# Performance work log

Hardware: AMD Instinct MI355X
Metric: run time of the kernel (lower is better)

Reference implementation:

```python
import jax, jax.numpy as jnp
import numpy as np

B = 64; SEQ = 512; PRED = 96; D = 321; HID = 2048
WIN = 64; STRIDE = WIN // 2; FT = WIN // 2 + 1
LOW = int(FT * 0.3); MID = int(FT * 0.4); HIGH = FT - LOW - MID  # 9, 13, 11
NW = SEQ // STRIDE + 1; EMBED = NW * WIN  # 17, 1088
EPS = 1e-5; SCALE = 0.02
LH = int(LOW * 2.0); MH = int(MID * 2.0); HH = int(HIGH * 2.0)  # 18, 26, 22


def _clayer(key, fan_in, fan_out):
    k1, k2, k3, k4 = jax.random.split(key, 4)
    return (jax.random.normal(k1, (fan_in, fan_out), jnp.float32) * SCALE,
            jax.random.normal(k2, (fan_in, fan_out), jnp.float32) * SCALE,
            jax.random.normal(k3, (fan_out,), jnp.float32) * SCALE,
            jax.random.normal(k4, (fan_out,), jnp.float32) * SCALE)


def setup_inputs() -> dict:
    key = jax.random.key(0)
    ks = jax.random.split(key, 12)
    inp = {}
    inp["x"] = jax.random.normal(ks[0], (B, SEQ, D), jnp.float32)
    inp["x_mark_enc"] = jax.random.normal(ks[1], (B, SEQ, 4), jnp.float32)
    inp["x_dec"] = jax.random.normal(ks[2], (B, PRED, D), jnp.float32)
    inp["x_mark_dec"] = jax.random.normal(ks[3], (B, PRED, 4), jnp.float32)
    n = jnp.arange(WIN, dtype=jnp.float32)
    inp["window"] = 0.5 * (1.0 - jnp.cos(2.0 * jnp.pi * n / WIN))  # torch.hann_window (periodic)
    inp["revin_w"] = jnp.ones((D,), jnp.float32)
    inp["revin_b"] = jnp.zeros((D,), jnp.float32)
    # low band filter: 3 complex layers LOW->LH->LH->LOW
    for i, (fi, fo) in enumerate([(LOW, LH), (LH, LH), (LH, LOW)]):
        wr, wi, br, bi = _clayer(jax.random.fold_in(ks[4], i), fi, fo)
        inp[f"low{i}_wr"], inp[f"low{i}_wi"], inp[f"low{i}_br"], inp[f"low{i}_bi"] = wr, wi, br, bi
    # mid band filter: 2 complex layers MID->MH->MID
    for i, (fi, fo) in enumerate([(MID, MH), (MH, MID)]):
        wr, wi, br, bi = _clayer(jax.random.fold_in(ks[5], i), fi, fo)
        inp[f"mid{i}_wr"], inp[f"mid{i}_wi"], inp[f"mid{i}_br"], inp[f"mid{i}_bi"] = wr, wi, br, bi
    # high band filter: 1 complex layer HIGH->HIGH
    wr, wi, br, bi = _clayer(ks[6], HIGH, HIGH)
    inp["high0_wr"], inp["high0_wi"], inp["high0_br"], inp["high0_bi"] = wr, wi, br, bi
    inp["fc1_w"] = jax.random.normal(ks[7], (EMBED, HID), jnp.float32) * SCALE
    inp["fc1_b"] = jnp.zeros((HID,), jnp.float32)
    inp["fc2_w"] = jax.random.normal(ks[8], (HID, PRED), jnp.float32) * SCALE
    inp["fc2_b"] = jnp.zeros((PRED,), jnp.float32)
    return inp


def _clin(z, wr, wi, br, bi):
    return z @ (wr + 1j * wi) + (br + 1j * bi)


def _cact(z):
    return jax.nn.leaky_relu(z.real) + 1j * jax.nn.leaky_relu(z.imag)


def reference(x, x_mark_enc, x_dec, x_mark_dec, window, revin_w, revin_b,
              low0_wr, low0_wi, low0_br, low0_bi,
              low1_wr, low1_wi, low1_br, low1_bi,
              low2_wr, low2_wi, low2_br, low2_bi,
              mid0_wr, mid0_wi, mid0_br, mid0_bi,
              mid1_wr, mid1_wi, mid1_br, mid1_bi,
              high0_wr, high0_wi, high0_br, high0_bi,
              fc1_w, fc1_b, fc2_w, fc2_b):
    # RevIN norm over time dim
    mean = jnp.mean(x, axis=1, keepdims=True)
    std = jnp.sqrt(jnp.var(x, axis=1, keepdims=True) + EPS)
    xn = (x - mean) / std * revin_w + revin_b
    xc = jnp.transpose(xn, (0, 2, 1))                      # [B, D, L]
    xp = jnp.pad(xc, ((0, 0), (0, 0), (STRIDE, STRIDE)))
    # batched window extraction (replaces python loop over windows)
    idx = jnp.arange(NW)[:, None] * STRIDE + jnp.arange(WIN)[None, :]
    seg = xp[:, :, idx]
    w = window / jnp.linalg.norm(window)
    xf = jnp.fft.rfft(seg * w, axis=-1)                    # [B, D, NW, FT] complex
    low = xf[..., :LOW]
    mid = xf[..., LOW:LOW + MID]
    high = xf[..., LOW + MID:]
    low = _clin(_cact(_clin(_cact(_clin(low, low0_wr, low0_wi, low0_br, low0_bi)),
                            low1_wr, low1_wi, low1_br, low1_bi)),
                low2_wr, low2_wi, low2_br, low2_bi)
    mid = _clin(_cact(_clin(mid, mid0_wr, mid0_wi, mid0_br, mid0_bi)),
                mid1_wr, mid1_wi, mid1_br, mid1_bi)
    high = _clin(high, high0_wr, high0_wi, high0_br, high0_bi)
    xfil = jnp.concatenate([low, mid, high], axis=-1)      # [B, D, NW, FT]
    xt = jnp.fft.irfft(xfil, n=WIN, axis=-1)
    emb = xt.reshape(x.shape[0], D, EMBED)
    h = jax.nn.leaky_relu(emb @ fc1_w + fc1_b)
    y = h @ fc2_w + fc2_b                                  # [B, D, PRED]
    y = jnp.transpose(y, (0, 2, 1))                        # [B, PRED, D]
    # RevIN denorm
    y = (y - revin_b) / (revin_w + EPS * EPS) * std + mean
    return y
```

## Files before the change

### kernel.cpp

```cpp
#include <hip/hip_runtime.h>

typedef unsigned short u16;
typedef unsigned int   u32;
typedef __attribute__((ext_vector_type(4))) float  fvec4;
typedef __attribute__((ext_vector_type(8))) __bf16 bvec8;

#define NB    64
#define SEQL  512
#define DCH   321
#define BDTOT (NB * DCH)
#define NWIN  17
#define PREDL 96
#define MWTOT (BDTOT * NWIN)

__device__ __forceinline__ u16 f2bf(float f) {
    union { float f; u32 u; } v; v.f = f;
    u32 r = v.u + 0x7FFFu + ((v.u >> 16) & 1u);
    return (u16)(r >> 16);
}
__device__ __forceinline__ float lrelu(float v) { return v > 0.f ? v : 0.01f * v; }

__device__ __forceinline__ void gld16(const u16* g, u16* l) {
    __builtin_amdgcn_global_load_lds((const __attribute__((address_space(1))) void*)g,
                                     (__attribute__((address_space(3))) void*)l, 16, 0, 0);
}

__global__ __launch_bounds__(256) void stats_kernel(const float* __restrict__ x,
                                                    float* __restrict__ mean,
                                                    float* __restrict__ rstd,
                                                    float* __restrict__ stdv) {
    __shared__ float ls[2][4][64];
    int i = threadIdx.x & 63;
    int j = threadIdx.x >> 6;
    int bd = blockIdx.x * 64 + i;
    int b = bd / DCH, d = bd - b * DCH;
    float s = 0.f, ss = 0.f;
    for (int t = j; t < SEQL; t += 4) {
        float v = x[((size_t)b * SEQL + t) * DCH + d];
        s += v; ss += v * v;
    }
    ls[0][j][i] = s; ls[1][j][i] = ss;
    __syncthreads();
    if (j == 0) {
        s  = ls[0][0][i] + ls[0][1][i] + ls[0][2][i] + ls[0][3][i];
        ss = ls[1][0][i] + ls[1][1][i] + ls[1][2][i] + ls[1][3][i];
        float m   = s * (1.f / SEQL);
        float var = ss * (1.f / SEQL) - m * m;
        float st  = sqrtf(var + 1e-5f);
        mean[bd] = m; rstd[bd] = 1.f / st; stdv[bd] = st;
    }
}

__global__ __launch_bounds__(256) void norm_transpose(const float* __restrict__ x,
                                                      const float* __restrict__ mean,
                                                      const float* __restrict__ rstd,
                                                      const float* __restrict__ rw,
                                                      const float* __restrict__ rb,
                                                      u16* __restrict__ xnT) {
    __shared__ float tile[64][65];
    int d0 = blockIdx.x * 64, s0 = blockIdx.y * 64, b = blockIdx.z;
    for (int e = threadIdx.x; e < 4096; e += 256) {
        int sr = e >> 6, dc = e & 63;
        int d = d0 + dc;
        tile[sr][dc] = (d < DCH) ? x[((size_t)b * SEQL + s0 + sr) * DCH + d] : 0.f;
    }
    __syncthreads();
    for (int e = threadIdx.x; e < 4096; e += 256) {
        int dr = e >> 6, sc = e & 63;
        int d = d0 + dr;
        if (d < DCH) {
            int bd = b * DCH + d;
            float v = (tile[sc][dr] - mean[bd]) * rstd[bd] * rw[d] + rb[d];
            xnT[(size_t)bd * 576 + 32 + s0 + sc] = f2bf(v);
        }
    }
}

__global__ __launch_bounds__(256) void pad_zero(u16* __restrict__ xnT) {
    int idx = blockIdx.x * 256 + threadIdx.x;
    if (idx < BDTOT * 64) {
        int bd = idx >> 6, q = idx & 63;
        int off = q < 32 ? q : 512 + q;
        xnT[(size_t)bd * 576 + off] = 0;
    }
}

__global__ __launch_bounds__(256) void precompute_kernel(
    const float* __restrict__ window,
    const float* __restrict__ l0wr, const float* __restrict__ l0wi,
    const float* __restrict__ l0br, const float* __restrict__ l0bi,
    const float* __restrict__ l1wr, const float* __restrict__ l1wi,
    const float* __restrict__ l1br, const float* __restrict__ l1bi,
    const float* __restrict__ l2wr, const float* __restrict__ l2wi,
    const float* __restrict__ l2br, const float* __restrict__ l2bi,
    const float* __restrict__ m0wr, const float* __restrict__ m0wi,
    const float* __restrict__ m0br, const float* __restrict__ m0bi,
    const float* __restrict__ m1wr, const float* __restrict__ m1wi,
    const float* __restrict__ m1br, const float* __restrict__ m1bi,
    const float* __restrict__ h0wr, const float* __restrict__ h0wi,
    const float* __restrict__ h0br, const float* __restrict__ h0bi,
    u16* __restrict__ A1t, u16* __restrict__ W1t, u16* __restrict__ B2t,
    float* __restrict__ bias1, float* __restrict__ bias2, float* __restrict__ biast)
{
    int idx = blockIdx.x * 256 + threadIdx.x;
    float nrm = 0.f;
    for (int i = 0; i < 64; ++i) nrm += window[i] * window[i];
    float inv = 1.0f / sqrtf(nrm);
    const float STEP = 6.283185307179586f / 64.f;
    auto Cc = [&](int n, int k) { return  window[n] * inv * cosf(STEP * (float)((k * n) & 63)); };
    auto Ss = [&](int n, int k) { return -window[n] * inv * sinf(STEP * (float)((k * n) & 63)); };
    auto aRe = [&](int k, int n) {
        float sc = (k == 0 || k == 32) ? (1.f / 64.f) : (2.f / 64.f);
        return sc * cosf(STEP * (float)((k * n) & 63));
    };
    auto aIm = [&](int k, int n) {
        if (k == 0 || k == 32) return 0.f;
        return -(2.f / 64.f) * sinf(STEP * (float)((k * n) & 63));
    };
    if (idx < 16384) {
        int j = idx >> 6, n = idx & 63;
        float v = 0.f;
        if (j < 18)                    { for (int k = 0; k < 9;  ++k) v += Cc(n,k)   *l0wr[k*18+j]      - Ss(n,k)   *l0wi[k*18+j]; }
        else if (j < 36)               { int jj=j-18; for (int k = 0; k < 9;  ++k) v += Cc(n,k)   *l0wi[k*18+jj] + Ss(n,k)   *l0wr[k*18+jj]; }
        else if (j >= 64  && j < 90)   { int jj=j-64; for (int k = 0; k < 13; ++k) v += Cc(n,9+k) *m0wr[k*26+jj] - Ss(n,9+k) *m0wi[k*26+jj]; }
        else if (j >= 90  && j < 116)  { int jj=j-90; for (int k = 0; k < 13; ++k) v += Cc(n,9+k) *m0wi[k*26+jj] + Ss(n,9+k) *m0wr[k*26+jj]; }
        else if (j >= 128 && j < 139)  { int jj=j-128;for (int k = 0; k < 11; ++k) v += Cc(n,22+k)*h0wr[k*11+jj] - Ss(n,22+k)*h0wi[k*11+jj]; }
        else if (j >= 139 && j < 150)  { int jj=j-139;for (int k = 0; k < 11; ++k) v += Cc(n,22+k)*h0wi[k*11+jj] + Ss(n,22+k)*h0wr[k*11+jj]; }
        A1t[idx] = f2bf(v);
    } else if (idx < 24576) {
        int t = idx - 16384; int j = t >> 6, k = t & 63;
        float v = 0.f;
        if (j < 18)      { if (k < 18) v = l1wr[k*18+j];        else if (k < 36) v = -l1wi[(k-18)*18+j]; }
        else if (j < 36) { int jj=j-18; if (k < 18) v = l1wi[k*18+jj]; else if (k < 36) v =  l1wr[(k-18)*18+jj]; }
        W1t[t] = f2bf(v);
    } else if (idx < 49152) {
        int t = idx - 24576; int n = t / 192, c = t - n * 192;
        float v = 0.f;
        if (n < 64) {
            if (c < 18)                  { for (int m = 0; m < 9;  ++m) v +=  l2wr[c*9+m]     *aRe(m,n)   + l2wi[c*9+m]     *aIm(m,n); }
            else if (c < 36)             { int cc=c-18; for (int m = 0; m < 9;  ++m) v += -l2wi[cc*9+m]   *aRe(m,n)   + l2wr[cc*9+m]   *aIm(m,n); }
            else if (c >= 64 && c < 90)  { int cc=c-64; for (int m = 0; m < 13; ++m) v +=  m1wr[cc*13+m]  *aRe(9+m,n) + m1wi[cc*13+m]  *aIm(9+m,n); }
            else if (c >= 90 && c < 116) { int cc=c-90; for (int m = 0; m < 13; ++m) v += -m1wi[cc*13+m]  *aRe(9+m,n) + m1wr[cc*13+m]  *aIm(9+m,n); }
            else if (c >= 128 && c < 139){ v = aRe(22 + (c-128), n); }
            else if (c >= 139 && c < 150){ v = aIm(22 + (c-139), n); }
        }
        B2t[t] = f2bf(v);
    } else if (idx < 49344) {
        int c = idx - 49152;
        float v = 0.f;
        if (c < 18) v = l0br[c];
        else if (c < 36) v = l0bi[c-18];
        else if (c >= 64 && c < 90) v = m0br[c-64];
        else if (c >= 90 && c < 116) v = m0bi[c-90];
        bias1[c] = v;
    } else if (idx < 49472) {
        int c = idx - 49344;
        float v = 0.f;
        if (c < 18) v = l1br[c]; else if (c < 36) v = l1bi[c-18];
        bias2[c] = v;
    } else if (idx < 49536) {
        int n = idx - 49472;
        float v = 0.f;
        for (int k = 0; k <= 32; ++k) {
            float br = (k < 9) ? l2br[k] : (k < 22 ? m1br[k-9] : h0br[k-22]);
            float bi = (k < 9) ? l2bi[k] : (k < 22 ? m1bi[k-9] : h0bi[k-22]);
            v += aRe(k, n) * br + aIm(k, n) * bi;
        }
        biast[n] = v;
    }
}

__global__ __launch_bounds__(256) void wtrans(const float* __restrict__ W, u16* __restrict__ Wt,
                                              int R, int C, int Cpad) {
    __shared__ float t[32][33];
    int c0 = blockIdx.x * 32, r0 = blockIdx.y * 32;
    for (int e = threadIdx.x; e < 1024; e += 256) {
        int rr = e >> 5, cc = e & 31;
        int rg = r0 + rr, cg = c0 + cc;
        t[rr][cc] = (rg < R && cg < C) ? W[(size_t)rg * C + cg] : 0.f;
    }
    __syncthreads();
    for (int e = threadIdx.x; e < 1024; e += 256) {
        int cr = e >> 5, rc = e & 31;
        int cg = c0 + cr, rg = r0 + rc;
        if (cg < Cpad && rg < R) Wt[(size_t)cg * R + rg] = f2bf(t[rc][cr]);
    }
}

__global__ __launch_bounds__(256) void spectral_fused(
    const u16* __restrict__ xnT, const u16* __restrict__ A1t,
    const u16* __restrict__ W1t, const u16* __restrict__ B2t,
    const float* __restrict__ bias1, const float* __restrict__ bias2,
    const float* __restrict__ biast, u16* __restrict__ EMB)
{
    __shared__ u16 XB[64 * 72];
    __shared__ u16 ACT[64 * 208];
    const int tid  = threadIdx.x;
    const int lane = tid & 63;
    const int wn   = tid >> 6;
    const int r0   = blockIdx.x * 64;

    {
        int rr = tid >> 2;
        int cc = (tid & 3) * 16;
        u32 gr = (u32)(r0 + rr);
        u32 bd = gr / 17u, nw = gr - bd * 17u;
        const u16* src = xnT + (size_t)bd * 576 + nw * 32 + cc;
        *(bvec8*)&XB[rr * 72 + cc]     = *(const bvec8*)(src);
        *(bvec8*)&XB[rr * 72 + cc + 8] = *(const bvec8*)(src + 8);
    }
    __syncthreads();

    fvec4 acc1[4][3] = {};
#pragma unroll
    for (int kk = 0; kk < 2; ++kk) {
        int ko = kk * 32 + ((lane >> 4) << 3);
        bvec8 af[4], bf[3];
#pragma unroll
        for (int m = 0; m < 4; ++m)
            af[m] = *(const bvec8*)&XB[(m * 16 + (lane & 15)) * 72 + ko];
#pragma unroll
        for (int n = 0; n < 3; ++n)
            bf[n] = *(const bvec8*)(A1t + (size_t)(wn * 48 + n * 16 + (lane & 15)) * 64 + ko);
#pragma unroll
        for (int m = 0; m < 4; ++m)
#pragma unroll
            for (int n = 0; n < 3; ++n)
                acc1[m][n] = __builtin_amdgcn_mfma_f32_16x16x32_bf16(af[m], bf[n], acc1[m][n], 0, 0, 0);
    }
#pragma unroll
    for (int n = 0; n < 3; ++n) {
        int col = wn * 48 + n * 16 + (lane & 15);
        float bs = bias1[col];
#pragma unroll
        for (int m = 0; m < 4; ++m)
#pragma unroll
            for (int q = 0; q < 4; ++q) {
                int row = m * 16 + ((lane >> 4) << 2) + q;
                float v = acc1[m][n][q] + bs;
                if (col < 128) v = lrelu(v);
                ACT[row * 208 + col] = f2bf(v);
            }
    }
    __syncthreads();

    fvec4 acc2[4] = {};
#pragma unroll
    for (int kk = 0; kk < 2; ++kk) {
        int ko = kk * 32 + ((lane >> 4) << 3);
        bvec8 bf = *(const bvec8*)(W1t + (size_t)(wn * 16 + (lane & 15)) * 64 + ko);
#pragma unroll
        for (int m = 0; m < 4; ++m) {
            bvec8 af = *(const bvec8*)&ACT[(m * 16 + (lane & 15)) * 208 + ko];
            acc2[m] = __builtin_amdgcn_mfma_f32_16x16x32_bf16(af, bf, acc2[m], 0, 0, 0);
        }
    }
    __syncthreads();
    {
        int col = wn * 16 + (lane & 15);
        float bs = bias2[col];
#pragma unroll
        for (int m = 0; m < 4; ++m)
#pragma unroll
            for (int q = 0; q < 4; ++q) {
                int row = m * 16 + ((lane >> 4) << 2) + q;
                ACT[row * 208 + col] = f2bf(lrelu(acc2[m][q] + bs));
            }
    }
    __syncthreads();

    fvec4 acc3[4] = {};
#pragma unroll
    for (int kk = 0; kk < 6; ++kk) {
        int ko = kk * 32 + ((lane >> 4) << 3);
        bvec8 bf = *(const bvec8*)(B2t + (size_t)(wn * 16 + (lane & 15)) * 192 + ko);
#pragma unroll
        for (int m = 0; m < 4; ++m) {
            bvec8 af = *(const bvec8*)&ACT[(m * 16 + (lane & 15)) * 208 + ko];
            acc3[m] = __builtin_amdgcn_mfma_f32_16x16x32_bf16(af, bf, acc3[m], 0, 0, 0);
        }
    }
    {
        int col = wn * 16 + (lane & 15);
        float bs = biast[col];
#pragma unroll
        for (int m = 0; m < 4; ++m)
#pragma unroll
            for (int q = 0; q < 4; ++q) {
                int row = m * 16 + ((lane >> 4) << 2) + q;
                EMB[(size_t)(r0 + row) * 64 + col] = f2bf(acc3[m][q] + bs);
            }
    }
}

template <int SWZ>
__global__ __launch_bounds__(512, 2) void gemm256(
    const u16* __restrict__ A, const u16* __restrict__ Bt,
    const float* __restrict__ bias, u16* __restrict__ C,
    int Mloc, int K, int ldc, long long a_off, int nwg)
{
    extern __shared__ u16 lds[];
    const int tid  = threadIdx.x;
    const int lane = tid & 63;
    const int wid  = tid >> 6;
    const int wm   = wid >> 2;
    const int wn   = wid & 3;
    int wg;
    if (SWZ) {
        int bid = blockIdx.x;
        int q = nwg >> 3, r = nwg & 7, xcd = bid & 7, off = bid >> 3;
        wg = (xcd < r) ? (xcd * (q + 1) + off) : (r * (q + 1) + (xcd - r) * q + off);
    } else wg = blockIdx.x;
    const int mt = wg >> 3;
    const int nt = wg & 7;
    const int bm0 = mt * 256, bn0 = nt * 256;

    auto stage = [&](int bufb, int kt) {
        u16* dstA = lds + bufb * 32768;
        u16* dstB = dstA + 16384;
#pragma unroll
        for (int j = 0; j < 4; ++j) {
            int idx = j * 512 + tid;
            int r  = idx >> 3;
            int kc = (idx & 7) << 3;
            int rl = bm0 + r; if (rl > Mloc - 1) rl = Mloc - 1;
            gld16(A  + (size_t)(a_off + rl) * K + kt + kc, dstA + idx * 8);
            gld16(Bt + (size_t)(bn0 + r)   * K + kt + kc, dstB + idx * 8);
        }
    };

    fvec4 acc[8][4] = {};

    auto compute = [&](int bufb) {
        const u16* Ab = lds + bufb * 32768;
        const u16* Bb = Ab + 16384;
        __builtin_amdgcn_s_setprio(1);
#pragma unroll
        for (int kk = 0; kk < 2; ++kk) {
            int ko = kk * 32 + ((lane >> 4) << 3);
            bvec8 af[8], bf[4];
#pragma unroll
            for (int m = 0; m < 8; ++m)
                af[m] = *(const bvec8*)&Ab[(wm * 128 + m * 16 + (lane & 15)) * 64 + ko];
#pragma unroll
            for (int n = 0; n < 4; ++n)
                bf[n] = *(const bvec8*)&Bb[(wn * 64 + n * 16 + (lane & 15)) * 64 + ko];
#pragma unroll
            for (int m = 0; m < 8; ++m)
#pragma unroll
                for (int n = 0; n < 4; ++n)
                    acc[m][n] = __builtin_amdgcn_mfma_f32_16x16x32_bf16(af[m], bf[n], acc[m][n], 0, 0, 0);
        }
        __builtin_amdgcn_s_setprio(0);
    };

    const int NT = K >> 6;
    stage(0, 0);
    int cur = 0;
    for (int t = 0; t < NT - 1; ++t) {
        stage(cur ^ 1, (t + 1) << 6);
        asm volatile("s_waitcnt vmcnt(8)" ::: "memory");
        __builtin_amdgcn_sched_barrier(0);
        __builtin_amdgcn_s_barrier();
        __builtin_amdgcn_sched_barrier(0);
        compute(cur);
        __builtin_amdgcn_sched_barrier(0);
        __builtin_amdgcn_s_barrier();
        __builtin_amdgcn_sched_barrier(0);
        cur ^= 1;
    }
    asm volatile("s_waitcnt vmcnt(0)" ::: "memory");
    __builtin_amdgcn_sched_barrier(0);
    __builtin_amdgcn_s_barrier();
    __builtin_amdgcn_sched_barrier(0);
    compute(cur);

#pragma unroll
    for (int m = 0; m < 8; ++m) {
        int rl0 = bm0 + wm * 128 + m * 16 + ((lane >> 4) << 2);
#pragma unroll
        for (int n = 0; n < 4; ++n) {
            int col = bn0 + wn * 64 + n * 16 + (lane & 15);
            float bs = bias[col];
#pragma unroll
            for (int q = 0; q < 4; ++q) {
                int rl = rl0 + q;
                if (rl < Mloc)
                    C[(size_t)rl * (size_t)ldc + col] = f2bf(lrelu(acc[m][n][q] + bs));
            }
        }
    }
}

__global__ __launch_bounds__(256) void gemm_bt_splitk(
    const u16* __restrict__ A, const u16* __restrict__ Bt,
    void* __restrict__ Cp, int Mloc, int N, int K, int lda, int ldc,
    long long c_off, int klen, long long pstride)
{
    const int tid  = threadIdx.x;
    const int lane = tid & 63;
    const int wm   = (tid >> 7) & 1;
    const int wn   = (tid >> 6) & 1;
    const int mt = blockIdx.y;
    int k0 = blockIdx.x * klen;
    int k1 = (k0 + klen > K) ? K : k0 + klen;
    const int bn0 = 0;
    const int bm0 = mt * 128;
    __shared__ u16 Als[128 * 64];
    __shared__ u16 Bls[128 * 64];
    fvec4 acc[4][4] = {};

    for (int kt = k0; kt < k1; kt += 64) {
#pragma unroll
        for (int i = 0; i < 4; ++i) {
            int idx = i * 256 + tid;
            int r  = idx >> 3;
            int kc = (idx & 7) << 3;
            int rl = bm0 + r; if (rl > Mloc - 1) rl = Mloc - 1;
            gld16(A + (size_t)rl * lda + kt + kc, &Als[idx * 8]);
            gld16(Bt + (size_t)(bn0 + r) * K + kt + kc, &Bls[idx * 8]);
        }
        __syncthreads();
#pragma unroll
        for (int kk = 0; kk < 2; ++kk) {
            int ko = kk * 32 + ((lane >> 4) << 3);
            bvec8 af[4], bfr[4];
#pragma unroll
            for (int m = 0; m < 4; ++m)
                af[m] = *(const bvec8*)&Als[(wm * 64 + m * 16 + (lane & 15)) * 64 + ko];
#pragma unroll
            for (int n = 0; n < 4; ++n)
                bfr[n] = *(const bvec8*)&Bls[(wn * 64 + n * 16 + (lane & 15)) * 64 + ko];
#pragma unroll
            for (int m = 0; m < 4; ++m)
#pragma unroll
                for (int n = 0; n < 4; ++n)
                    acc[m][n] = __builtin_amdgcn_mfma_f32_16x16x32_bf16(af[m], bfr[n], acc[m][n], 0, 0, 0);
        }
        __syncthreads();
    }

#pragma unroll
    for (int m = 0; m < 4; ++m) {
        int rbase = bm0 + wm * 64 + m * 16 + ((lane >> 4) << 2);
#pragma unroll
        for (int n = 0; n < 4; ++n) {
            int col = bn0 + wn * 64 + n * 16 + (lane & 15);
            if (col < N) {
#pragma unroll
                for (int q = 0; q < 4; ++q) {
                    int rl = rbase + q;
                    if (rl < Mloc) {
                        float* yp = (float*)Cp + (size_t)blockIdx.x * pstride;
                        yp[(size_t)(c_off + rl) * ldc + col] = acc[m][n][q];
                    }
                }
            }
        }
    }
}

__global__ __launch_bounds__(256) void final_denorm(const float* __restrict__ YP,
                                                    const float* __restrict__ fc2b,
                                                    const float* __restrict__ mean,
                                                    const float* __restrict__ stdv,
                                                    const float* __restrict__ rw,
                                                    const float* __restrict__ rb,
                                                    float* __restrict__ out) {
    const long long PART = (long long)BDTOT * PREDL;
    __shared__ float t[32][33];
    int d0 = blockIdx.x * 32, p0 = blockIdx.y * 32, b = blockIdx.z;
    for (int e = threadIdx.x; e < 1024; e += 256) {
        int di = e >> 5, pj = e & 31;
        int d = d0 + di, p = p0 + pj;
        if (d < DCH && p < PREDL) {
            size_t off = ((size_t)b * DCH + d) * PREDL + p;
            t[di][pj] = YP[off] + YP[off + PART] + YP[off + 2 * PART] + fc2b[p];
        } else t[di][pj] = 0.f;
    }
    __syncthreads();
    for (int e = threadIdx.x; e < 1024; e += 256) {
        int pi = e >> 5, dj = e & 31;
        int d = d0 + dj, p = p0 + pi;
        if (d < DCH && p < PREDL) {
            int bd = b * DCH + d;
            float v = (t[dj][pi] - rb[d]) / (rw[d] + 1e-10f) * stdv[bd] + mean[bd];
            out[((size_t)b * PREDL + p) * DCH + d] = v;
        }
    }
}

extern "C" void kernel_launch(void* const* d_in, const int* in_sizes, int n_in,
                              void* d_out, int out_size, void* d_ws, size_t ws_size,
                              hipStream_t stream) {
    const float* x      = (const float*)d_in[0];
    const float* window = (const float*)d_in[4];
    const float* rw     = (const float*)d_in[5];
    const float* rb     = (const float*)d_in[6];
    const float* l0wr = (const float*)d_in[7],  *l0wi = (const float*)d_in[8];
    const float* l0br = (const float*)d_in[9],  *l0bi = (const float*)d_in[10];
    const float* l1wr = (const float*)d_in[11], *l1wi = (const float*)d_in[12];
    const float* l1br = (const float*)d_in[13], *l1bi = (const float*)d_in[14];
    const float* l2wr = (const float*)d_in[15], *l2wi = (const float*)d_in[16];
    const float* l2br = (const float*)d_in[17], *l2bi = (const float*)d_in[18];
    const float* m0wr = (const float*)d_in[19], *m0wi = (const float*)d_in[20];
    const float* m0br = (const float*)d_in[21], *m0bi = (const float*)d_in[22];
    const float* m1wr = (const float*)d_in[23], *m1wi = (const float*)d_in[24];
    const float* m1br = (const float*)d_in[25], *m1bi = (const float*)d_in[26];
    const float* h0wr = (const float*)d_in[27], *h0wi = (const float*)d_in[28];
    const float* h0br = (const float*)d_in[29], *h0bi = (const float*)d_in[30];
    const float* fc1w = (const float*)d_in[31];
    const float* fc1b = (const float*)d_in[32];
    const float* fc2w = (const float*)d_in[33];
    const float* fc2b = (const float*)d_in[34];

    char* p = (char*)d_ws;
    auto alloc = [&](size_t n) { char* r = p; p += (n + 255) & ~(size_t)255; return r; };
    float* mean  = (float*)alloc(BDTOT * 4);
    float* rstd  = (float*)alloc(BDTOT * 4);
    float* stdv  = (float*)alloc(BDTOT * 4);
    float* bias1 = (float*)alloc(192 * 4);
    float* bias2 = (float*)alloc(128 * 4);
    float* biast = (float*)alloc(64 * 4);
    u16* A1t   = (u16*)alloc(256 * 64 * 2);
    u16* W1t   = (u16*)alloc(128 * 64 * 2);
    u16* B2t   = (u16*)alloc(128 * 192 * 2);
    u16* fc1wT = (u16*)alloc((size_t)2048 * 1088 * 2);
    u16* fc2wT = (u16*)alloc((size_t)128 * 2048 * 2);
    u16* xnT   = (u16*)alloc((size_t)BDTOT * 576 * 2);
    float* YP  = (float*)xnT;
    u16* EMB   = (u16*)alloc((size_t)BDTOT * 1088 * 2);

    size_t fixed_end = (size_t)(p - (char*)d_ws);
    int CH = 16;
    const int chs[5] = {1, 2, 4, 8, 16};
    for (int ci = 0; ci < 5; ++ci) {
        int c = chs[ci];
        size_t hbuf = (size_t)(BDTOT / c) * 2048 * 2;
        if (fixed_end + hbuf <= ws_size) { CH = c; break; }
    }
    int bd_c = BDTOT / CH;
    u16* Hbuf = (u16*)p;

    hipFuncSetAttribute(reinterpret_cast<const void*>(&gemm256<1>),
                        hipFuncAttributeMaxDynamicSharedMemorySize, 131072);

    dim3 blk(256);
    stats_kernel<<<BDTOT / 64, blk, 0, stream>>>(x, mean, rstd, stdv);
    norm_transpose<<<dim3(6, 8, NB), blk, 0, stream>>>(x, mean, rstd, rw, rb, xnT);
    pad_zero<<<(BDTOT * 64 + 255) / 256, blk, 0, stream>>>(xnT);
    precompute_kernel<<<194, blk, 0, stream>>>(window,
        l0wr, l0wi, l0br, l0bi, l1wr, l1wi, l1br, l1bi, l2wr, l2wi, l2br, l2bi,
        m0wr, m0wi, m0br, m0bi, m1wr, m1wi, m1br, m1bi, h0wr, h0wi, h0br, h0bi,
        A1t, W1t, B2t, bias1, bias2, biast);
    wtrans<<<dim3(64, 34), blk, 0, stream>>>(fc1w, fc1wT, 1088, 2048, 2048);
    wtrans<<<dim3(4, 64),  blk, 0, stream>>>(fc2w, fc2wT, 2048, 96, 128);

    spectral_fused<<<MWTOT / 64, blk, 0, stream>>>(xnT, A1t, W1t, B2t, bias1, bias2, biast, EMB);

    const long long PART = (long long)BDTOT * PREDL;
    for (int c = 0; c < CH; ++c) {
        long long boff = (long long)c * bd_c;
        int gm = (bd_c + 255) / 256;
        int nwg = 8 * gm;
        gemm256<1><<<dim3(nwg), dim3(512), 131072, stream>>>(EMB, fc1wT, fc1b, Hbuf,
            bd_c, 1088, 2048, boff, nwg);
        gemm_bt_splitk<<<dim3(3, (bd_c + 127) / 128), blk, 0, stream>>>(Hbuf, fc2wT, YP,
            bd_c, 96, 2048, 2048, 96, boff, 704, PART);
    }
    final_denorm<<<dim3(11, 3, NB), blk, 0, stream>>>(YP, fc2b, mean, stdv, rw, rb, (float*)d_out);
}
```

Baseline: 347.5 us.

## Restructure fc1 GEMM into phased pipeline with XOR-swizzled LDS and padded K

```diff
diff --git a/kernel.cpp b/kernel.cpp
--- a/kernel.cpp
+++ b/kernel.cpp
@@ -12,6 +12,7 @@
 #define NWIN  17
 #define PREDL 96
 #define MWTOT (BDTOT * NWIN)
+#define KPAD  1152
 
 __device__ __forceinline__ u16 f2bf(float f) {
     union { float f; u32 u; } v; v.f = f;
@@ -82,6 +83,15 @@
         int bd = idx >> 6, q = idx & 63;
         int off = q < 32 ? q : 512 + q;
         xnT[(size_t)bd * 576 + off] = 0;
+    }
+}
+
+__global__ __launch_bounds__(256) void pad_emb(u16* __restrict__ EMB) {
+    int idx = blockIdx.x * 256 + threadIdx.x;
+    if (idx < BDTOT * 8) {
+        int bd = idx >> 3, o = (idx & 7) * 8;
+        fvec4 z = {0.f, 0.f, 0.f, 0.f};
+        *(fvec4*)&EMB[(size_t)bd * KPAD + 1088 + o] = z;
     }
 }
 
@@ -171,7 +181,7 @@
 }
 
 __global__ __launch_bounds__(256) void wtrans(const float* __restrict__ W, u16* __restrict__ Wt,
-                                              int R, int C, int Cpad) {
+                                              int R, int C, int Cpad, int ldw) {
     __shared__ float t[32][33];
     int c0 = blockIdx.x * 32, r0 = blockIdx.y * 32;
     for (int e = threadIdx.x; e < 1024; e += 256) {
@@ -183,7 +193,7 @@
     for (int e = threadIdx.x; e < 1024; e += 256) {
         int cr = e >> 5, rc = e & 31;
         int cg = c0 + cr, rg = r0 + rc;
-        if (cg < Cpad && rg < R) Wt[(size_t)cg * R + rg] = f2bf(t[rc][cr]);
+        if (cg < Cpad && rg < ldw) Wt[(size_t)cg * ldw + rg] = f2bf(t[rc][cr]);
     }
 }
 
@@ -288,13 +298,15 @@
 #pragma unroll
             for (int q = 0; q < 4; ++q) {
                 int row = m * 16 + ((lane >> 4) << 2) + q;
-                EMB[(size_t)(r0 + row) * 64 + col] = f2bf(acc3[m][q] + bs);
+                int wr = r0 + row;
+                int bd2 = wr / 17, nw2 = wr - bd2 * 17;
+                EMB[(size_t)bd2 * KPAD + nw2 * 64 + col] = f2bf(acc3[m][q] + bs);
             }
     }
 }
 
 template <int SWZ>
-__global__ __launch_bounds__(512, 2) void gemm256(
+__global__ __launch_bounds__(512, 2) void gemm256_8ph(
     const u16* __restrict__ A, const u16* __restrict__ Bt,
     const float* __restrict__ bias, u16* __restrict__ C,
     int Mloc, int K, int ldc, long long a_off, int nwg)
@@ -302,6 +314,8 @@
     extern __shared__ u16 lds[];
     const int tid  = threadIdx.x;
     const int lane = tid & 63;
+    const int l15  = lane & 15;
+    const int hi   = lane >> 4;
     const int wid  = tid >> 6;
     const int wm   = wid >> 2;
     const int wn   = wid & 3;
@@ -315,72 +329,94 @@
     const int nt = wg & 7;
     const int bm0 = mt * 256, bn0 = nt * 256;
 
-    auto stage = [&](int bufb, int kt) {
-        u16* dstA = lds + bufb * 32768;
-        u16* dstB = dstA + 16384;
-#pragma unroll
-        for (int j = 0; j < 4; ++j) {
+    const u16* sbase[4][2];
+#pragma unroll
+    for (int u = 0; u < 4; ++u) {
+        const int mat = u >> 1, half = u & 1;
+#pragma unroll
+        for (int j = 0; j < 2; ++j) {
             int idx = j * 512 + tid;
-            int r  = idx >> 3;
-            int kc = (idx & 7) << 3;
-            int rl = bm0 + r; if (rl > Mloc - 1) rl = Mloc - 1;
-            gld16(A  + (size_t)(a_off + rl) * K + kt + kc, dstA + idx * 8);
-            gld16(Bt + (size_t)(bn0 + r)   * K + kt + kc, dstB + idx * 8);
+            int row = half * 128 + (idx >> 3);
+            int kc = ((idx & 7) ^ (row & 7)) << 3;
+            if (mat == 0) {
+                int rl = bm0 + row; if (rl > Mloc - 1) rl = Mloc - 1;
+                sbase[u][j] = A + (size_t)(a_off + rl) * K + kc;
+            } else {
+                sbase[u][j] = Bt + (size_t)(bn0 + row) * K + kc;
+            }
+        }
+    }
+    auto stage_unit = [&](int bufb, int tg, int u) {
+        const int mat = u >> 1, half = u & 1;
+        u16* dstb = lds + bufb * 32768 + mat * 16384 + half * 8192;
+#pragma unroll
+        for (int j = 0; j < 2; ++j) {
+            int idx = j * 512 + tid;
+            gld16(sbase[u][j] + ((size_t)tg << 6), dstb + idx * 8);
         }
     };
 
     fvec4 acc[8][4] = {};
-
-    auto compute = [&](int bufb) {
-        const u16* Ab = lds + bufb * 32768;
-        const u16* Bb = Ab + 16384;
-        __builtin_amdgcn_s_setprio(1);
-#pragma unroll
-        for (int kk = 0; kk < 2; ++kk) {
-            int ko = kk * 32 + ((lane >> 4) << 3);
-            bvec8 af[8], bf[4];
-#pragma unroll
-            for (int m = 0; m < 8; ++m)
-                af[m] = *(const bvec8*)&Ab[(wm * 128 + m * 16 + (lane & 15)) * 64 + ko];
-#pragma unroll
-            for (int n = 0; n < 4; ++n)
-                bf[n] = *(const bvec8*)&Bb[(wn * 64 + n * 16 + (lane & 15)) * 64 + ko];
-#pragma unroll
-            for (int m = 0; m < 8; ++m)
-#pragma unroll
-                for (int n = 0; n < 4; ++n)
-                    acc[m][n] = __builtin_amdgcn_mfma_f32_16x16x32_bf16(af[m], bf[n], acc[m][n], 0, 0, 0);
-        }
-        __builtin_amdgcn_s_setprio(0);
-    };
-
     const int NT = K >> 6;
-    stage(0, 0);
-    int cur = 0;
-    for (int t = 0; t < NT - 1; ++t) {
-        stage(cur ^ 1, (t + 1) << 6);
-        asm volatile("s_waitcnt vmcnt(8)" ::: "memory");
-        __builtin_amdgcn_sched_barrier(0);
-        __builtin_amdgcn_s_barrier();
-        __builtin_amdgcn_sched_barrier(0);
-        compute(cur);
-        __builtin_amdgcn_sched_barrier(0);
-        __builtin_amdgcn_s_barrier();
-        __builtin_amdgcn_sched_barrier(0);
-        cur ^= 1;
-    }
+
+#pragma unroll
+    for (int u = 0; u < 4; ++u) stage_unit(0, 0, u);
     asm volatile("s_waitcnt vmcnt(0)" ::: "memory");
     __builtin_amdgcn_sched_barrier(0);
     __builtin_amdgcn_s_barrier();
     __builtin_amdgcn_sched_barrier(0);
-    compute(cur);
+
+    for (int t = 0; t < NT; ++t) {
+        const int cur = t & 1;
+        const u16* Ab = lds + cur * 32768;
+        const u16* Bb = Ab + 16384;
+        const bool notlast = (t < NT - 1);
+        bvec8 bfr[4];
+#pragma unroll
+        for (int p = 0; p < 4; ++p) {
+            const int kk = p >> 1, mh = p & 1;
+            bvec8 af[4];
+            if (mh == 0) {
+#pragma unroll
+                for (int n = 0; n < 4; ++n) {
+                    int r = wn * 64 + n * 16 + l15;
+                    int bc = (kk * 4 + hi) ^ (l15 & 7);
+                    bfr[n] = *(const bvec8*)&Bb[r * 64 + bc * 8];
+                }
+            }
+#pragma unroll
+            for (int mm = 0; mm < 4; ++mm) {
+                int r = wm * 128 + (mh * 4 + mm) * 16 + l15;
+                int bc = (kk * 4 + hi) ^ (l15 & 7);
+                af[mm] = *(const bvec8*)&Ab[r * 64 + bc * 8];
+            }
+            if (notlast) stage_unit(cur ^ 1, t + 1, p);
+            __builtin_amdgcn_sched_barrier(0);
+            __builtin_amdgcn_s_barrier();
+            __builtin_amdgcn_sched_barrier(0);
+            __builtin_amdgcn_s_setprio(1);
+#pragma unroll
+            for (int mm = 0; mm < 4; ++mm)
+#pragma unroll
+                for (int n = 0; n < 4; ++n)
+                    acc[mh * 4 + mm][n] = __builtin_amdgcn_mfma_f32_16x16x32_bf16(
+                        af[mm], bfr[n], acc[mh * 4 + mm][n], 0, 0, 0);
+            __builtin_amdgcn_s_setprio(0);
+            if (p == 3) {
+                asm volatile("s_waitcnt vmcnt(0)" ::: "memory");
+            }
+            __builtin_amdgcn_sched_barrier(0);
+            __builtin_amdgcn_s_barrier();
+            __builtin_amdgcn_sched_barrier(0);
+        }
+    }
 
 #pragma unroll
     for (int m = 0; m < 8; ++m) {
         int rl0 = bm0 + wm * 128 + m * 16 + ((lane >> 4) << 2);
 #pragma unroll
         for (int n = 0; n < 4; ++n) {
-            int col = bn0 + wn * 64 + n * 16 + (lane & 15);
+            int col = bn0 + wn * 64 + n * 16 + l15;
             float bs = bias[col];
 #pragma unroll
             for (int q = 0; q < 4; ++q) {
@@ -525,11 +561,11 @@
     u16* A1t   = (u16*)alloc(256 * 64 * 2);
     u16* W1t   = (u16*)alloc(128 * 64 * 2);
     u16* B2t   = (u16*)alloc(128 * 192 * 2);
-    u16* fc1wT = (u16*)alloc((size_t)2048 * 1088 * 2);
+    u16* fc1wT = (u16*)alloc((size_t)2048 * KPAD * 2);
     u16* fc2wT = (u16*)alloc((size_t)128 * 2048 * 2);
     u16* xnT   = (u16*)alloc((size_t)BDTOT * 576 * 2);
     float* YP  = (float*)xnT;
-    u16* EMB   = (u16*)alloc((size_t)BDTOT * 1088 * 2);
+    u16* EMB   = (u16*)alloc((size_t)BDTOT * KPAD * 2);
 
     size_t fixed_end = (size_t)(p - (char*)d_ws);
     int CH = 16;
@@ -542,7 +578,7 @@
     int bd_c = BDTOT / CH;
     u16* Hbuf = (u16*)p;
 
-    hipFuncSetAttribute(reinterpret_cast<const void*>(&gemm256<1>),
+    hipFuncSetAttribute(reinterpret_cast<const void*>(&gemm256_8ph<1>),
                         hipFuncAttributeMaxDynamicSharedMemorySize, 131072);
 
     dim3 blk(256);
@@ -553,18 +589,19 @@
         l0wr, l0wi, l0br, l0bi, l1wr, l1wi, l1br, l1bi, l2wr, l2wi, l2br, l2bi,
         m0wr, m0wi, m0br, m0bi, m1wr, m1wi, m1br, m1bi, h0wr, h0wi, h0br, h0bi,
         A1t, W1t, B2t, bias1, bias2, biast);
-    wtrans<<<dim3(64, 34), blk, 0, stream>>>(fc1w, fc1wT, 1088, 2048, 2048);
-    wtrans<<<dim3(4, 64),  blk, 0, stream>>>(fc2w, fc2wT, 2048, 96, 128);
+    wtrans<<<dim3(64, 36), blk, 0, stream>>>(fc1w, fc1wT, 1088, 2048, 2048, KPAD);
+    wtrans<<<dim3(4, 64),  blk, 0, stream>>>(fc2w, fc2wT, 2048, 96, 128, 2048);
 
     spectral_fused<<<MWTOT / 64, blk, 0, stream>>>(xnT, A1t, W1t, B2t, bias1, bias2, biast, EMB);
+    pad_emb<<<(BDTOT * 8 + 255) / 256, blk, 0, stream>>>(EMB);
 
     const long long PART = (long long)BDTOT * PREDL;
     for (int c = 0; c < CH; ++c) {
         long long boff = (long long)c * bd_c;
         int gm = (bd_c + 255) / 256;
         int nwg = 8 * gm;
-        gemm256<1><<<dim3(nwg), dim3(512), 131072, stream>>>(EMB, fc1wT, fc1b, Hbuf,
-            bd_c, 1088, 2048, boff, nwg);
+        gemm256_8ph<1><<<dim3(nwg), dim3(512), 131072, stream>>>(EMB, fc1wT, fc1b, Hbuf,
+            bd_c, KPAD, 2048, boff, nwg);
         gemm_bt_splitk<<<dim3(3, (bd_c + 127) / 128), blk, 0, stream>>>(Hbuf, fc2wT, YP,
             bd_c, 96, 2048, 2048, 96, boff, 704, PART);
     }
```

Result: faster. 321.3 us (-7.6%).
